# Kernel tuning notes

Hardware: AMD Instinct MI355X
Metric: run time of the kernel (lower is better)

Reference implementation:

```python
import jax, jax.numpy as jnp
import numpy as np

B, S, D, H = 4, 2048, 1024, 16
HD = D // H  # head_length = 64


def setup_inputs() -> dict:
    key = jax.random.key(0)
    ks = jax.random.split(key, 11)
    s = 1.0 / np.sqrt(D)
    return {
        "queries": jax.random.normal(ks[0], (B, S, D), jnp.float32),
        "keys": jax.random.normal(ks[1], (B, S, D), jnp.float32),
        "values": jax.random.normal(ks[2], (B, S, D), jnp.float32),
        "Wq": jax.random.normal(ks[3], (D, D), jnp.float32) * s,
        "bq": jnp.zeros((D,), jnp.float32),
        "Wk": jax.random.normal(ks[4], (D, D), jnp.float32) * s,
        "bk": jnp.zeros((D,), jnp.float32),
        "Wv": jax.random.normal(ks[5], (D, D), jnp.float32) * s,
        "bv": jnp.zeros((D,), jnp.float32),
        "Wo": jax.random.normal(ks[6], (D, D), jnp.float32) * s,
        "bo": jnp.zeros((D,), jnp.float32),
    }


def reference(queries, keys, values, Wq, bq, Wk, bk, Wv, bv, Wo, bo):
    # Linear projections (torch Linear: x @ W^T + b), split into heads -> [B, H, S, HD]
    def proj(x, W, b):
        return (x @ W.T + b).reshape(B, S, H, HD).transpose(0, 2, 1, 3)

    q = proj(queries, Wq, bq)
    k = proj(keys, Wk, bk)
    v = proj(values, Wv, bv)
    # Scaled dot-product attention, scale = 1/sqrt(head_length)
    scores = jnp.einsum("bhsd,bhtd->bhst", q, k) / jnp.sqrt(jnp.float32(HD))
    attn = jax.nn.softmax(scores, axis=-1)
    out = jnp.einsum("bhst,bhtd->bhsd", attn, v)  # [B, H, S, HD]
    out = out.transpose(0, 2, 1, 3).reshape(B, S, D)
    return out @ Wo.T + bo
```

## Files before the change

### kernel.cpp

```cpp
#include <hip/hip_runtime.h>
#include <stdint.h>
#include <stddef.h>

#define B_ 4
#define S_ 2048
#define D_ 1024
#define H_ 16
#define HD_ 64

#define QSCALE 0.18033688f

typedef __bf16 bf16;
typedef __bf16 bf16x8 __attribute__((ext_vector_type(8)));
typedef __bf16 bf16x4 __attribute__((ext_vector_type(4)));
typedef float f32x4 __attribute__((ext_vector_type(4)));
typedef float f32x16 __attribute__((ext_vector_type(16)));
typedef uint32_t u32x4 __attribute__((ext_vector_type(4)));

__device__ __forceinline__ f32x4 mfma16(bf16x8 a, bf16x8 b, f32x4 c) {
  return __builtin_amdgcn_mfma_f32_16x16x32_bf16(a, b, c, 0, 0, 0);
}
__device__ __forceinline__ f32x16 mfma32(bf16x8 a, bf16x8 b, f32x16 c) {
  return __builtin_amdgcn_mfma_f32_32x32x16_bf16(a, b, c, 0, 0, 0);
}

__device__ __forceinline__ float fexp2(float x) {
#if __has_builtin(__builtin_amdgcn_exp2f)
  return __builtin_amdgcn_exp2f(x);
#else
  return exp2f(x);
#endif
}

__device__ __forceinline__ void gload_lds16(const void* g, void* l) {
  __builtin_amdgcn_global_load_lds(
      (__attribute__((address_space(1))) uint32_t*)(uintptr_t)g,
      (__attribute__((address_space(3))) uint32_t*)l, 16, 0, 0);
}

__device__ __forceinline__ uint32_t cvt_pk(float lo, float hi) {
  uint32_t r;
  asm volatile("v_cvt_pk_bf16_f32 %0, %1, %2" : "=v"(r) : "v"(lo), "v"(hi));
  return r;
}

__device__ __forceinline__ void pl_swap(uint32_t& a, uint32_t& b) {
#if __has_builtin(__builtin_amdgcn_permlane32_swap)
  typedef int i32x2_t __attribute__((ext_vector_type(2)));
  i32x2_t r = __builtin_amdgcn_permlane32_swap((int)a, (int)b, false, false);
  a = (uint32_t)r[0];
  b = (uint32_t)r[1];
#else
  uint32_t pa_ = (uint32_t)__shfl_xor((int)a, 32);
  uint32_t pb_ = (uint32_t)__shfl_xor((int)b, 32);
  bool hi_ = (threadIdx.x & 32) != 0;
  uint32_t na = hi_ ? pb_ : a;
  uint32_t nb = hi_ ? b : pa_;
  a = na;
  b = nb;
#endif
}

__device__ __forceinline__ bf16x8 pack4(uint32_t a, uint32_t b, uint32_t c,
                                        uint32_t d) {
  u32x4 v = {a, b, c, d};
  return __builtin_bit_cast(bf16x8, v);
}

__global__ __launch_bounds__(256) void convert_w(
    const float* __restrict__ a, const float* __restrict__ b,
    const float* __restrict__ c, const float* __restrict__ d,
    bf16* __restrict__ out) {
  int i = (blockIdx.x * 256 + threadIdx.x) * 4;
  const float* srcs[4] = {a, b, c, d};
#pragma unroll
  for (int w = 0; w < 4; ++w) {
    f32x4 x = *(const f32x4*)(srcs[w] + i);
    bf16x4 v;
    v[0] = (bf16)x[0]; v[1] = (bf16)x[1]; v[2] = (bf16)x[2]; v[3] = (bf16)x[3];
    *(bf16x4*)(out + (size_t)w * (D_ * D_) + i) = v;
  }
}

__global__ __launch_bounds__(256) void convert_in(const float* __restrict__ in,
                                                  bf16* __restrict__ out) {
  const int n8 = (B_ * S_ * D_) / 8;
  for (int i = blockIdx.x * 256 + threadIdx.x; i < n8; i += gridDim.x * 256) {
    f32x4 x0 = *(const f32x4*)(in + (size_t)i * 8);
    f32x4 x1 = *(const f32x4*)(in + (size_t)i * 8 + 4);
    bf16x8 v;
    v[0] = (bf16)x0[0]; v[1] = (bf16)x0[1]; v[2] = (bf16)x0[2]; v[3] = (bf16)x0[3];
    v[4] = (bf16)x1[0]; v[5] = (bf16)x1[1]; v[6] = (bf16)x1[2]; v[7] = (bf16)x1[3];
    *(bf16x8*)(out + (size_t)i * 8) = v;
  }
}

template <int MODE>
__global__ __launch_bounds__(256, 2) void gemm_bf16(
    const bf16* __restrict__ A, const bf16* __restrict__ Wb,
    const float* __restrict__ bias, void* __restrict__ Out, float oscale) {
  __shared__ alignas(128) char lds[32768];
  const int tid = threadIdx.x;
  const int lane = tid & 63;
  const int wave = tid >> 6;
  const int m0 = blockIdx.x * 128;
  const int n0 = blockIdx.y * 128;
  const int wr = wave >> 1, wc = wave & 1;

  f32x4 acc[4][4] = {};

  for (int kt = 0; kt < 16; ++kt) {
    const int k0 = kt * 64;
#pragma unroll
    for (int j = 0; j < 4; ++j) {
      int slot = j * 256 + tid;
      int row = slot >> 3, kb = slot & 7;
      gload_lds16(A + (size_t)(m0 + row) * D_ + k0 + ((kb ^ (row & 7)) << 3),
                  lds + j * 4096 + wave * 1024);
    }
#pragma unroll
    for (int j = 0; j < 4; ++j) {
      int slot = j * 256 + tid;
      int row = slot >> 3, kb = slot & 7;
      gload_lds16(Wb + (size_t)(n0 + row) * D_ + k0 + ((kb ^ (row & 7)) << 3),
                  lds + 16384 + j * 4096 + wave * 1024);
    }
    __syncthreads();
#pragma unroll
    for (int ks = 0; ks < 2; ++ks) {
      bf16x8 af[4], bfr[4];
#pragma unroll
      for (int f = 0; f < 4; ++f) {
        int ar = wr * 64 + f * 16 + (lane & 15);
        af[f] = *(const bf16x8*)(lds + ar * 128 +
                                 (((ks * 4 + (lane >> 4)) ^ (ar & 7)) << 4));
        int br = wc * 64 + f * 16 + (lane & 15);
        bfr[f] = *(const bf16x8*)(lds + 16384 + br * 128 +
                                  (((ks * 4 + (lane >> 4)) ^ (br & 7)) << 4));
      }
#pragma unroll
      for (int i = 0; i < 4; ++i)
#pragma unroll
        for (int j = 0; j < 4; ++j)
          acc[i][j] = mfma16(af[i], bfr[j], acc[i][j]);
    }
    __syncthreads();
  }

#pragma unroll
  for (int j = 0; j < 4; ++j) {
    const int col = n0 + wc * 64 + j * 16 + (lane & 15);
    const float bv_ = bias[col];
    const int h = col >> 6, hd = col & 63;
#pragma unroll
    for (int i = 0; i < 4; ++i) {
      const int row0 = m0 + wr * 64 + i * 16 + ((lane >> 4) << 2);
      if (MODE == 2) {
        float* O = (float*)Out;
#pragma unroll
        for (int r = 0; r < 4; ++r)
          O[(size_t)(row0 + r) * D_ + col] = acc[i][j][r] + bv_;
      } else if (MODE == 0) {
        bf16* O = (bf16*)Out;
#pragma unroll
        for (int r = 0; r < 4; ++r) {
          int row = row0 + r;
          int b = row >> 11, s = row & (S_ - 1);
          O[(((size_t)(b * H_ + h) * S_ + s) << 6) + hd] =
              (bf16)((acc[i][j][r] + bv_) * oscale);
        }
      } else {
        bf16* O = (bf16*)Out;
        int b = row0 >> 11, s0 = row0 & (S_ - 1);
        bf16x4 pk;
#pragma unroll
        for (int r = 0; r < 4; ++r) pk[r] = (bf16)(acc[i][j][r] + bv_);
        *(bf16x4*)(O + ((size_t)(b * H_ + h) * HD_ + hd) * S_ + s0) = pk;
      }
    }
  }
}

__global__ __launch_bounds__(256, 2) void attn_kernel(
    const bf16* __restrict__ Qh, const bf16* __restrict__ Kh,
    const bf16* __restrict__ Vt, bf16* __restrict__ AO) {
  __shared__ alignas(128) char lds[2][16384];
  const int tid = threadIdx.x, lane = tid & 63, wave = tid >> 6;
  const int hi = lane >> 5, l31 = lane & 31;
  const int bh = blockIdx.y;
  const int q0 = blockIdx.x * 256 + wave * 64;
  const bf16* Qb = Qh + (size_t)bh * S_ * HD_;
  const bf16* Kb = Kh + (size_t)bh * S_ * HD_;
  const bf16* Vb = Vt + (size_t)bh * HD_ * S_;

  bf16x8 qf[2][4];
#pragma unroll
  for (int qg = 0; qg < 2; ++qg)
#pragma unroll
    for (int ks = 0; ks < 4; ++ks)
      qf[qg][ks] = *(const bf16x8*)(Qb + (size_t)(q0 + qg * 32 + l31) * HD_ +
                                    ks * 16 + hi * 8);

  bf16x8 onesf;
#pragma unroll
  for (int j = 0; j < 8; ++j) onesf[j] = (bf16)1.0f;

  const bf16* gs[4];
  int lo_[4], ginc[4];
#pragma unroll
  for (int j = 0; j < 4; ++j) {
    int f = j * 4 + wave;
    lo_[j] = f * 1024;
    if (f < 8) {
      gs[j] = Kb + (size_t)((f >> 2) * 32 + l31) * HD_ + (f & 3) * 16 + hi * 8;
      ginc[j] = 64 * HD_;
    } else {
      int g = f - 8;
      gs[j] = Vb + (size_t)((g & 1) * 32 + l31) * S_ + (g >> 1) * 16 + hi * 8;
      ginc[j] = 64;
    }
  }

  f32x16 oacc0[2] = {}, oacc1[2] = {};
  f32x16 dacc0 = {}, dacc1 = {};

#pragma unroll
  for (int j = 0; j < 4; ++j) {
    gload_lds16(gs[j], &lds[0][lo_[j]]);
    gs[j] += ginc[j];
  }
  __syncthreads();

  for (int t = 0; t < 32; ++t) {
    const int cur = t & 1;
    if (t < 31) {
#pragma unroll
      for (int j = 0; j < 4; ++j) {
        gload_lds16(gs[j], &lds[cur ^ 1][lo_[j]]);
        gs[j] += ginc[j];
      }
    }
    const char* kbuf = lds[cur];
    const char* vbuf = lds[cur] + 8192;
#pragma unroll
    for (int kb = 0; kb < 2; ++kb) {
      f32x16 s0 = {}, s1 = {};
      __builtin_amdgcn_s_setprio(1);
#pragma unroll
      for (int ks = 0; ks < 4; ++ks) {
        bf16x8 kf = *(const bf16x8*)(kbuf + (kb * 4 + ks) * 1024 + lane * 16);
        s0 = mfma32(kf, qf[0][ks], s0);
        s1 = mfma32(kf, qf[1][ks], s1);
      }
      __builtin_amdgcn_s_setprio(0);
      bf16x8 pa[2][2];
#pragma unroll
      for (int qg = 0; qg < 2; ++qg) {
        f32x16 s = qg ? s1 : s0;
        f32x16 e;
#pragma unroll
        for (int r = 0; r < 16; ++r) e[r] = fexp2(s[r]);
        uint32_t w0 = cvt_pk(e[0], e[1]), w1 = cvt_pk(e[2], e[3]),
                 w2 = cvt_pk(e[4], e[5]), w3 = cvt_pk(e[6], e[7]),
                 w4 = cvt_pk(e[8], e[9]), w5 = cvt_pk(e[10], e[11]),
                 w6 = cvt_pk(e[12], e[13]), w7 = cvt_pk(e[14], e[15]);
        pl_swap(w0, w2);
        pl_swap(w1, w3);
        pl_swap(w4, w6);
        pl_swap(w5, w7);
        pa[qg][0] = pack4(w0, w1, w2, w3);
        pa[qg][1] = pack4(w4, w5, w6, w7);
      }
      __builtin_amdgcn_s_setprio(1);
      dacc0 = mfma32(pa[0][0], onesf, dacc0);
      dacc0 = mfma32(pa[0][1], onesf, dacc0);
      dacc1 = mfma32(pa[1][0], onesf, dacc1);
      dacc1 = mfma32(pa[1][1], onesf, dacc1);
#pragma unroll
      for (int ht = 0; ht < 2; ++ht) {
        bf16x8 vf0 =
            *(const bf16x8*)(vbuf + ((kb * 2 + 0) * 2 + ht) * 1024 + lane * 16);
        oacc0[ht] = mfma32(pa[0][0], vf0, oacc0[ht]);
        oacc1[ht] = mfma32(pa[1][0], vf0, oacc1[ht]);
        bf16x8 vf1 =
            *(const bf16x8*)(vbuf + ((kb * 2 + 1) * 2 + ht) * 1024 + lane * 16);
        oacc0[ht] = mfma32(pa[0][1], vf1, oacc0[ht]);
        oacc1[ht] = mfma32(pa[1][1], vf1, oacc1[ht]);
      }
      __builtin_amdgcn_s_setprio(0);
    }
    __syncthreads();
  }

  const int b = bh >> 4, h = bh & 15;
#pragma unroll
  for (int qg = 0; qg < 2; ++qg) {
#pragma unroll
    for (int r = 0; r < 16; ++r) {
      float rd = 1.0f / (qg ? dacc1[r] : dacc0[r]);
      int qr = (r & 3) + 8 * (r >> 2) + 4 * hi;
      size_t base = ((size_t)(b * S_ + q0 + qg * 32 + qr)) * D_ + h * 64;
      AO[base + l31] = (bf16)((qg ? oacc1[0][r] : oacc0[0][r]) * rd);
      AO[base + 32 + l31] = (bf16)((qg ? oacc1[1][r] : oacc0[1][r]) * rd);
    }
  }
}

extern "C" void kernel_launch(void* const* d_in, const int* in_sizes, int n_in,
                              void* d_out, int out_size, void* d_ws,
                              size_t ws_size, hipStream_t stream) {
  (void)in_sizes; (void)n_in; (void)out_size; (void)ws_size;
  const float* q  = (const float*)d_in[0];
  const float* k  = (const float*)d_in[1];
  const float* v  = (const float*)d_in[2];
  const float* Wq = (const float*)d_in[3];
  const float* bq = (const float*)d_in[4];
  const float* Wk = (const float*)d_in[5];
  const float* bk = (const float*)d_in[6];
  const float* Wv = (const float*)d_in[7];
  const float* bv = (const float*)d_in[8];
  const float* Wo = (const float*)d_in[9];
  const float* bo = (const float*)d_in[10];

  bf16* ws = (bf16*)d_ws;
  const size_t WSZ = (size_t)D_ * D_;
  const size_t TSZ = (size_t)B_ * S_ * D_;
  bf16* Wqb = ws;
  bf16* Wkb = ws + WSZ;
  bf16* Wvb = ws + 2 * WSZ;
  bf16* Wob = ws + 3 * WSZ;
  bf16* Abf = ws + 4 * WSZ;
  bf16* Qh  = Abf + TSZ;
  bf16* Kh  = Qh + TSZ;
  bf16* Vt  = Kh + TSZ;
  bf16* AO  = Abf;

  convert_w<<<dim3(1024), dim3(256), 0, stream>>>(Wq, Wk, Wv, Wo, ws);
  dim3 gg(64, 8), bb(256);
  convert_in<<<dim3(2048), bb, 0, stream>>>(q, Abf);
  gemm_bf16<0><<<gg, bb, 0, stream>>>(Abf, Wqb, bq, Qh, QSCALE);
  convert_in<<<dim3(2048), bb, 0, stream>>>(k, Abf);
  gemm_bf16<0><<<gg, bb, 0, stream>>>(Abf, Wkb, bk, Kh, 1.0f);
  convert_in<<<dim3(2048), bb, 0, stream>>>(v, Abf);
  gemm_bf16<1><<<gg, bb, 0, stream>>>(Abf, Wvb, bv, Vt, 1.0f);
  attn_kernel<<<dim3(8, 64), bb, 0, stream>>>(Qh, Kh, Vt, AO);
  gemm_bf16<2><<<gg, bb, 0, stream>>>(AO, Wob, bo, d_out, 1.0f);
}
```

Before: 205.6 us.

## Halve per-wave query tile in attention, compute row sums on VALU, raise occupancy

Each wave of the attention kernel now handles 32 query rows instead of 64, and the grid becomes 1024 one-dimensional blocks with bh as the fast index, so blocks sharing a head run together. The softmax denominator is accumulated with scalar adds plus a cross-half shuffle instead of extra MFMAs against a ones vector. Launch bounds rise to 4 blocks per CU to exploit the lower register use. The cost is that each K/V tile loaded into LDS is reused by half as many query rows, so total K/V traffic and LDS reads per unit of MFMA work double.

```diff
diff --git a/kernel.cpp b/kernel.cpp
--- a/kernel.cpp
+++ b/kernel.cpp
@@ -181,29 +181,24 @@
   }
 }
 
-__global__ __launch_bounds__(256, 2) void attn_kernel(
+__global__ __launch_bounds__(256, 4) void attn_kernel(
     const bf16* __restrict__ Qh, const bf16* __restrict__ Kh,
     const bf16* __restrict__ Vt, bf16* __restrict__ AO) {
   __shared__ alignas(128) char lds[2][16384];
   const int tid = threadIdx.x, lane = tid & 63, wave = tid >> 6;
   const int hi = lane >> 5, l31 = lane & 31;
-  const int bh = blockIdx.y;
-  const int q0 = blockIdx.x * 256 + wave * 64;
+  const int bid = blockIdx.x;
+  const int bh = bid & 63;
+  const int qb = bid >> 6;
+  const int q0 = qb * 128 + wave * 32;
   const bf16* Qb = Qh + (size_t)bh * S_ * HD_;
   const bf16* Kb = Kh + (size_t)bh * S_ * HD_;
   const bf16* Vb = Vt + (size_t)bh * HD_ * S_;
 
-  bf16x8 qf[2][4];
-#pragma unroll
-  for (int qg = 0; qg < 2; ++qg)
-#pragma unroll
-    for (int ks = 0; ks < 4; ++ks)
-      qf[qg][ks] = *(const bf16x8*)(Qb + (size_t)(q0 + qg * 32 + l31) * HD_ +
-                                    ks * 16 + hi * 8);
-
-  bf16x8 onesf;
-#pragma unroll
-  for (int j = 0; j < 8; ++j) onesf[j] = (bf16)1.0f;
+  bf16x8 qf[4];
+#pragma unroll
+  for (int ks = 0; ks < 4; ++ks)
+    qf[ks] = *(const bf16x8*)(Qb + (size_t)(q0 + l31) * HD_ + ks * 16 + hi * 8);
 
   const bf16* gs[4];
   int lo_[4], ginc[4];
@@ -221,8 +216,8 @@
     }
   }
 
-  f32x16 oacc0[2] = {}, oacc1[2] = {};
-  f32x16 dacc0 = {}, dacc1 = {};
+  f32x16 oacc[2] = {};
+  float dl = 0.f;
 
 #pragma unroll
   for (int j = 0; j < 4; ++j) {
@@ -244,65 +239,59 @@
     const char* vbuf = lds[cur] + 8192;
 #pragma unroll
     for (int kb = 0; kb < 2; ++kb) {
-      f32x16 s0 = {}, s1 = {};
+      f32x16 s = {};
       __builtin_amdgcn_s_setprio(1);
 #pragma unroll
       for (int ks = 0; ks < 4; ++ks) {
         bf16x8 kf = *(const bf16x8*)(kbuf + (kb * 4 + ks) * 1024 + lane * 16);
-        s0 = mfma32(kf, qf[0][ks], s0);
-        s1 = mfma32(kf, qf[1][ks], s1);
+        s = mfma32(kf, qf[ks], s);
       }
       __builtin_amdgcn_s_setprio(0);
-      bf16x8 pa[2][2];
-#pragma unroll
-      for (int qg = 0; qg < 2; ++qg) {
-        f32x16 s = qg ? s1 : s0;
-        f32x16 e;
-#pragma unroll
-        for (int r = 0; r < 16; ++r) e[r] = fexp2(s[r]);
-        uint32_t w0 = cvt_pk(e[0], e[1]), w1 = cvt_pk(e[2], e[3]),
-                 w2 = cvt_pk(e[4], e[5]), w3 = cvt_pk(e[6], e[7]),
-                 w4 = cvt_pk(e[8], e[9]), w5 = cvt_pk(e[10], e[11]),
-                 w6 = cvt_pk(e[12], e[13]), w7 = cvt_pk(e[14], e[15]);
-        pl_swap(w0, w2);
-        pl_swap(w1, w3);
-        pl_swap(w4, w6);
-        pl_swap(w5, w7);
-        pa[qg][0] = pack4(w0, w1, w2, w3);
-        pa[qg][1] = pack4(w4, w5, w6, w7);
-      }
+      float e[16];
+#pragma unroll
+      for (int r = 0; r < 16; ++r) e[r] = fexp2(s[r]);
+      {
+        float a0 = e[0] + e[1], a1 = e[2] + e[3], a2 = e[4] + e[5],
+              a3 = e[6] + e[7], a4 = e[8] + e[9], a5 = e[10] + e[11],
+              a6 = e[12] + e[13], a7 = e[14] + e[15];
+        float b0 = a0 + a1, b1 = a2 + a3, b2 = a4 + a5, b3 = a6 + a7;
+        dl += (b0 + b1) + (b2 + b3);
+      }
+      uint32_t w0 = cvt_pk(e[0], e[1]), w1 = cvt_pk(e[2], e[3]),
+               w2 = cvt_pk(e[4], e[5]), w3 = cvt_pk(e[6], e[7]),
+               w4 = cvt_pk(e[8], e[9]), w5 = cvt_pk(e[10], e[11]),
+               w6 = cvt_pk(e[12], e[13]), w7 = cvt_pk(e[14], e[15]);
+      pl_swap(w0, w2);
+      pl_swap(w1, w3);
+      pl_swap(w4, w6);
+      pl_swap(w5, w7);
+      bf16x8 pa0 = pack4(w0, w1, w2, w3);
+      bf16x8 pa1 = pack4(w4, w5, w6, w7);
       __builtin_amdgcn_s_setprio(1);
-      dacc0 = mfma32(pa[0][0], onesf, dacc0);
-      dacc0 = mfma32(pa[0][1], onesf, dacc0);
-      dacc1 = mfma32(pa[1][0], onesf, dacc1);
-      dacc1 = mfma32(pa[1][1], onesf, dacc1);
 #pragma unroll
       for (int ht = 0; ht < 2; ++ht) {
         bf16x8 vf0 =
             *(const bf16x8*)(vbuf + ((kb * 2 + 0) * 2 + ht) * 1024 + lane * 16);
-        oacc0[ht] = mfma32(pa[0][0], vf0, oacc0[ht]);
-        oacc1[ht] = mfma32(pa[1][0], vf0, oacc1[ht]);
+        oacc[ht] = mfma32(pa0, vf0, oacc[ht]);
         bf16x8 vf1 =
             *(const bf16x8*)(vbuf + ((kb * 2 + 1) * 2 + ht) * 1024 + lane * 16);
-        oacc0[ht] = mfma32(pa[0][1], vf1, oacc0[ht]);
-        oacc1[ht] = mfma32(pa[1][1], vf1, oacc1[ht]);
+        oacc[ht] = mfma32(pa1, vf1, oacc[ht]);
       }
       __builtin_amdgcn_s_setprio(0);
     }
     __syncthreads();
   }
 
+  dl += __shfl_xor(dl, 32);
+  float rden = 1.0f / dl;
   const int b = bh >> 4, h = bh & 15;
 #pragma unroll
-  for (int qg = 0; qg < 2; ++qg) {
-#pragma unroll
-    for (int r = 0; r < 16; ++r) {
-      float rd = 1.0f / (qg ? dacc1[r] : dacc0[r]);
-      int qr = (r & 3) + 8 * (r >> 2) + 4 * hi;
-      size_t base = ((size_t)(b * S_ + q0 + qg * 32 + qr)) * D_ + h * 64;
-      AO[base + l31] = (bf16)((qg ? oacc1[0][r] : oacc0[0][r]) * rd);
-      AO[base + 32 + l31] = (bf16)((qg ? oacc1[1][r] : oacc0[1][r]) * rd);
-    }
+  for (int r = 0; r < 16; ++r) {
+    int qr = (r & 3) + 8 * (r >> 2) + 4 * hi;
+    float dr = __shfl(rden, qr);
+    size_t base = ((size_t)(b * S_ + q0 + qr)) * D_ + h * 64;
+    AO[base + l31] = (bf16)(oacc[0][r] * dr);
+    AO[base + 32 + l31] = (bf16)(oacc[1][r] * dr);
   }
 }
 
@@ -343,6 +332,6 @@
   gemm_bf16<0><<<gg, bb, 0, stream>>>(Abf, Wkb, bk, Kh, 1.0f);
   convert_in<<<dim3(2048), bb, 0, stream>>>(v, Abf);
   gemm_bf16<1><<<gg, bb, 0, stream>>>(Abf, Wvb, bv, Vt, 1.0f);
-  attn_kernel<<<dim3(8, 64), bb, 0, stream>>>(Qh, Kh, Vt, AO);
+  attn_kernel<<<dim3(1024), bb, 0, stream>>>(Qh, Kh, Vt, AO);
   gemm_bf16<2><<<gg, bb, 0, stream>>>(AO, Wob, bo, d_out, 1.0f);
 }
```

Result: no change. 204.0 us (-0.8%).

## Use 2-wave attention blocks and compute softmax denominators with VALU adds

Applied to the files above, without the earlier changes.

Attention blocks shrink from 4 waves to 2, giving 1024 blocks in a 1D grid with head index varying fastest. Each wave now issues twice as many K/V async loads per tile. The row-sum denominator is now accumulated with scalar adds on the fp32 exponentials plus shuffles at the end, replacing the extra MFMAs against a ones vector. This cuts matrix-core work and spreads blocks more evenly across CUs, at the cost of each K/V tile being shared by fewer waves, which raises total global-to-LDS traffic.

```diff
diff --git a/kernel.cpp b/kernel.cpp
--- a/kernel.cpp
+++ b/kernel.cpp
@@ -181,14 +181,16 @@
   }
 }
 
-__global__ __launch_bounds__(256, 2) void attn_kernel(
+__global__ __launch_bounds__(128, 2) void attn_kernel(
     const bf16* __restrict__ Qh, const bf16* __restrict__ Kh,
     const bf16* __restrict__ Vt, bf16* __restrict__ AO) {
   __shared__ alignas(128) char lds[2][16384];
   const int tid = threadIdx.x, lane = tid & 63, wave = tid >> 6;
   const int hi = lane >> 5, l31 = lane & 31;
-  const int bh = blockIdx.y;
-  const int q0 = blockIdx.x * 256 + wave * 64;
+  const int bid = blockIdx.x;
+  const int bh = bid & 63;
+  const int qb = bid >> 6;
+  const int q0 = qb * 128 + wave * 64;
   const bf16* Qb = Qh + (size_t)bh * S_ * HD_;
   const bf16* Kb = Kh + (size_t)bh * S_ * HD_;
   const bf16* Vb = Vt + (size_t)bh * HD_ * S_;
@@ -201,15 +203,11 @@
       qf[qg][ks] = *(const bf16x8*)(Qb + (size_t)(q0 + qg * 32 + l31) * HD_ +
                                     ks * 16 + hi * 8);
 
-  bf16x8 onesf;
-#pragma unroll
-  for (int j = 0; j < 8; ++j) onesf[j] = (bf16)1.0f;
-
-  const bf16* gs[4];
-  int lo_[4], ginc[4];
-#pragma unroll
-  for (int j = 0; j < 4; ++j) {
-    int f = j * 4 + wave;
+  const bf16* gs[8];
+  int lo_[8], ginc[8];
+#pragma unroll
+  for (int j = 0; j < 8; ++j) {
+    int f = j * 2 + wave;
     lo_[j] = f * 1024;
     if (f < 8) {
       gs[j] = Kb + (size_t)((f >> 2) * 32 + l31) * HD_ + (f & 3) * 16 + hi * 8;
@@ -221,11 +219,11 @@
     }
   }
 
-  f32x16 oacc0[2] = {}, oacc1[2] = {};
-  f32x16 dacc0 = {}, dacc1 = {};
-
-#pragma unroll
-  for (int j = 0; j < 4; ++j) {
+  f32x16 oacc[2][2] = {};
+  float dl[2] = {0.f, 0.f};
+
+#pragma unroll
+  for (int j = 0; j < 8; ++j) {
     gload_lds16(gs[j], &lds[0][lo_[j]]);
     gs[j] += ginc[j];
   }
@@ -235,7 +233,7 @@
     const int cur = t & 1;
     if (t < 31) {
 #pragma unroll
-      for (int j = 0; j < 4; ++j) {
+      for (int j = 0; j < 8; ++j) {
         gload_lds16(gs[j], &lds[cur ^ 1][lo_[j]]);
         gs[j] += ginc[j];
       }
@@ -257,9 +255,16 @@
 #pragma unroll
       for (int qg = 0; qg < 2; ++qg) {
         f32x16 s = qg ? s1 : s0;
-        f32x16 e;
+        float e[16];
 #pragma unroll
         for (int r = 0; r < 16; ++r) e[r] = fexp2(s[r]);
+        {
+          float a0 = e[0] + e[1], a1 = e[2] + e[3], a2 = e[4] + e[5],
+                a3 = e[6] + e[7], a4 = e[8] + e[9], a5 = e[10] + e[11],
+                a6 = e[12] + e[13], a7 = e[14] + e[15];
+          float b0 = a0 + a1, b1 = a2 + a3, b2 = a4 + a5, b3 = a6 + a7;
+          dl[qg] += (b0 + b1) + (b2 + b3);
+        }
         uint32_t w0 = cvt_pk(e[0], e[1]), w1 = cvt_pk(e[2], e[3]),
                  w2 = cvt_pk(e[4], e[5]), w3 = cvt_pk(e[6], e[7]),
                  w4 = cvt_pk(e[8], e[9]), w5 = cvt_pk(e[10], e[11]),
@@ -272,20 +277,16 @@
         pa[qg][1] = pack4(w4, w5, w6, w7);
       }
       __builtin_amdgcn_s_setprio(1);
-      dacc0 = mfma32(pa[0][0], onesf, dacc0);
-      dacc0 = mfma32(pa[0][1], onesf, dacc0);
-      dacc1 = mfma32(pa[1][0], onesf, dacc1);
-      dacc1 = mfma32(pa[1][1], onesf, dacc1);
 #pragma unroll
       for (int ht = 0; ht < 2; ++ht) {
         bf16x8 vf0 =
             *(const bf16x8*)(vbuf + ((kb * 2 + 0) * 2 + ht) * 1024 + lane * 16);
-        oacc0[ht] = mfma32(pa[0][0], vf0, oacc0[ht]);
-        oacc1[ht] = mfma32(pa[1][0], vf0, oacc1[ht]);
+        oacc[0][ht] = mfma32(pa[0][0], vf0, oacc[0][ht]);
+        oacc[1][ht] = mfma32(pa[1][0], vf0, oacc[1][ht]);
         bf16x8 vf1 =
             *(const bf16x8*)(vbuf + ((kb * 2 + 1) * 2 + ht) * 1024 + lane * 16);
-        oacc0[ht] = mfma32(pa[0][1], vf1, oacc0[ht]);
-        oacc1[ht] = mfma32(pa[1][1], vf1, oacc1[ht]);
+        oacc[0][ht] = mfma32(pa[0][1], vf1, oacc[0][ht]);
+        oacc[1][ht] = mfma32(pa[1][1], vf1, oacc[1][ht]);
       }
       __builtin_amdgcn_s_setprio(0);
     }
@@ -295,13 +296,15 @@
   const int b = bh >> 4, h = bh & 15;
 #pragma unroll
   for (int qg = 0; qg < 2; ++qg) {
+    float d = dl[qg] + __shfl_xor(dl[qg], 32);
+    float rden = 1.0f / d;
 #pragma unroll
     for (int r = 0; r < 16; ++r) {
-      float rd = 1.0f / (qg ? dacc1[r] : dacc0[r]);
       int qr = (r & 3) + 8 * (r >> 2) + 4 * hi;
+      float dr = __shfl(rden, qr);
       size_t base = ((size_t)(b * S_ + q0 + qg * 32 + qr)) * D_ + h * 64;
-      AO[base + l31] = (bf16)((qg ? oacc1[0][r] : oacc0[0][r]) * rd);
-      AO[base + 32 + l31] = (bf16)((qg ? oacc1[1][r] : oacc0[1][r]) * rd);
+      AO[base + l31] = (bf16)(oacc[qg][0][r] * dr);
+      AO[base + 32 + l31] = (bf16)(oacc[qg][1][r] * dr);
     }
   }
 }
@@ -343,6 +346,6 @@
   gemm_bf16<0><<<gg, bb, 0, stream>>>(Abf, Wkb, bk, Kh, 1.0f);
   convert_in<<<dim3(2048), bb, 0, stream>>>(v, Abf);
   gemm_bf16<1><<<gg, bb, 0, stream>>>(Abf, Wvb, bv, Vt, 1.0f);
-  attn_kernel<<<dim3(8, 64), bb, 0, stream>>>(Qh, Kh, Vt, AO);
+  attn_kernel<<<dim3(1024), dim3(128), 0, stream>>>(Qh, Kh, Vt, AO);
   gemm_bf16<2><<<gg, bb, 0, stream>>>(AO, Wob, bo, d_out, 1.0f);
 }
```

After: 205.8 us. Within noise of the previous version (+0.1%).
